# Optimization experiments

Hardware: AMD Instinct MI355X
Metric: run time of the kernel (lower is better)

## Reference

```python
import jax, jax.numpy as jnp
import numpy as np

MAX_ITERS = 20
TOL = 1e-6
STEP = 1.0
EPS = 1e-7
CLIP = 1e-7


def _normalize(x, axis=-1):
    n = jnp.linalg.norm(x, axis=axis, keepdims=True)
    return x / jnp.maximum(n, 1e-12)


def _safe_acos(x):
    return jnp.arccos(jnp.clip(x, -1.0 + CLIP, 1.0 - CLIP))


def setup_inputs() -> dict:
    key = jax.random.key(0)
    NC, K, N, D = 1000, 8, 32, 128
    X_groups = jax.random.normal(key, (NC, K, N, D), dtype=jnp.float32)
    return {"X_groups": X_groups}


def reference(X_groups):
    # X_groups: (NC, K, N, D)
    NC, K, N, D = X_groups.shape
    X = X_groups.reshape(NC * K, N, D)
    Xn = _normalize(X)                      # (G, N, D) unit vectors
    mu = _normalize(jnp.mean(Xn, axis=1))   # (G, D) init mean

    done = jnp.array(False)
    for _ in range(MAX_ITERS):
        dots = jnp.einsum('gd,gnd->gn', mu, Xn)             # (G, N)
        theta = _safe_acos(dots)
        sin_t = jnp.maximum(jnp.sin(theta), EPS)
        diff = Xn - dots[..., None] * mu[:, None, :]        # (G, N, D)
        log_vecs = (theta / sin_t)[..., None] * diff        # log map
        v = jnp.mean(log_vecs, axis=1)                      # (G, D)
        v_norm = jnp.maximum(jnp.linalg.norm(v, axis=-1, keepdims=True), EPS)
        done = done | (jnp.max(v_norm) < TOL)               # global convergence (as in torch .item() check)
        v_step = STEP * v
        vs_norm = jnp.maximum(jnp.linalg.norm(v_step, axis=-1, keepdims=True), EPS)
        mu_new = jnp.cos(vs_norm) * mu + jnp.sin(vs_norm) * (v_step / vs_norm)  # exp map
        mu_new = _normalize(mu_new)
        mu = jnp.where(done, mu, mu_new)

    # calc_cluster_distance: features (G, N, D) @ means (G, D)
    sims = jnp.einsum('gnd,gd->gn', Xn, mu)
    sims = jnp.clip(sims, -1 + CLIP, 1 - CLIP)
    loss = jnp.mean(jnp.sum(jnp.arccos(sims) ** 2, axis=-1))
    return loss
```

## Files before the change

kernel.cpp:

```cpp
#include <hip/hip_runtime.h>
#include <stdint.h>

#define MAX_ITERS 20
#define EPSV 1e-7f
#define CLIPV 1e-7f
#define PI_F 3.14159265358979f
#define PIO2_F 1.57079632679490f

typedef __attribute__((ext_vector_type(8))) short short8;
typedef __attribute__((ext_vector_type(4))) float f4;

__device__ __forceinline__ f4 mfma_bf16(short8 a, short8 b, f4 c) {
    return __builtin_amdgcn_mfma_f32_16x16x32_bf16(a, b, c, 0, 0, 0);
}

__device__ __forceinline__ float rl(float v, int l) {
    return __int_as_float(__builtin_amdgcn_readlane(__float_as_int(v), l));
}

template <int CTRL>
__device__ __forceinline__ float dpp_add(float v) {
    int p = __builtin_amdgcn_update_dpp(0, __float_as_int(v), CTRL, 0xF, 0xF, true);
    return v + __int_as_float(p);
}

__device__ __forceinline__ float rowsum32(float v) {
    v = dpp_add<0xB1>(v);
    v = dpp_add<0x4E>(v);
    v = dpp_add<0x141>(v);
    v = dpp_add<0x140>(v);
    return rl(v, 0) + rl(v, 16);
}

__device__ __forceinline__ float fast_acos(float x) {
    float a = fabsf(x);
    bool big = a > 0.5f;
    float z = big ? 0.5f * (1.0f - a) : x * x;
    float s = big ? sqrtf(z) : x;
    float p = fmaf(z, fmaf(z, fmaf(z, fmaf(z, 4.2163199048e-2f, 2.4181311049e-2f),
                                   4.5470025998e-2f), 7.4953002686e-2f),
                   1.6666752422e-1f);
    float r = fmaf(s * z, p, s);
    float big_val = (x < 0.0f) ? (PI_F - 2.0f * r) : (2.0f * r);
    return big ? big_val : (PIO2_F - r);
}

__device__ __forceinline__ void cvt_hilo(const float* v, short8& hi, short8& lo) {
#pragma unroll
    for (int i = 0; i < 8; ++i) {
        float x = v[i];
        uint32_t u = __float_as_uint(x);
        float hf = __uint_as_float(u & 0xFFFF0000u);
        float lf = x - hf;
        hi[i] = (short)(u >> 16);
        lo[i] = (short)(__float_as_uint(lf) >> 16);
    }
}

__global__ void __launch_bounds__(256) karcher(const float* __restrict__ X,
                                               float* __restrict__ ws,
                                               int n_groups) {
    __shared__ float sG[4][32 * 33];
    __shared__ float sInv[4][32];
    __shared__ float sPart[4];

    const int lane = threadIdx.x & 63;
    const int wid  = threadIdx.x >> 6;
    const int g    = blockIdx.x * 4 + wid;
    if (g >= n_groups) return;

    const float* Xg = X + (size_t)g * (32 * 128);
    const int col  = lane & 15;
    const int quad = lane >> 4;

    f4 acc00 = {0.f, 0.f, 0.f, 0.f};
    f4 acc01 = acc00, acc10 = acc00, acc11 = acc00;
#pragma unroll
    for (int kc = 0; kc < 4; ++kc) {
        const float* p0 = Xg + col * 128 + kc * 32 + quad * 8;
        const float* p1 = p0 + 16 * 128;
        float r0[8], r1[8];
        *(float4*)(r0)     = *(const float4*)(p0);
        *(float4*)(r0 + 4) = *(const float4*)(p0 + 4);
        *(float4*)(r1)     = *(const float4*)(p1);
        *(float4*)(r1 + 4) = *(const float4*)(p1 + 4);
        short8 H0, L0, H1, L1;
        cvt_hilo(r0, H0, L0);
        cvt_hilo(r1, H1, L1);
        acc00 = mfma_bf16(H0, H0, acc00);
        acc00 = mfma_bf16(H0, L0, acc00);
        acc00 = mfma_bf16(L0, H0, acc00);
        acc01 = mfma_bf16(H0, H1, acc01);
        acc01 = mfma_bf16(H0, L1, acc01);
        acc01 = mfma_bf16(L0, H1, acc01);
        acc10 = mfma_bf16(H1, H0, acc10);
        acc10 = mfma_bf16(H1, L0, acc10);
        acc10 = mfma_bf16(L1, H0, acc10);
        acc11 = mfma_bf16(H1, H1, acc11);
        acc11 = mfma_bf16(H1, L1, acc11);
        acc11 = mfma_bf16(L1, H1, acc11);
    }

    float* Gw = sG[wid];
#pragma unroll
    for (int i = 0; i < 4; ++i) {
        int rw = quad * 4 + i;
        Gw[rw * 33 + col]             = acc00[i];
        Gw[rw * 33 + col + 16]        = acc01[i];
        Gw[(rw + 16) * 33 + col]      = acc10[i];
        Gw[(rw + 16) * 33 + col + 16] = acc11[i];
    }
    __syncthreads();

    const int r = lane & 31;
    {
        float d = Gw[r * 33 + r];
        sInv[wid][r] = 1.0f / fmaxf(sqrtf(d), 1e-12f);
    }
    __syncthreads();

    float Grow[32];
    {
        float invr = sInv[wid][r];
#pragma unroll
        for (int j = 0; j < 32; ++j)
            Grow[j] = Gw[r * 33 + j] * (invr * sInv[wid][j]);
    }

    float a = 1.0f / 32.0f;
    float ga;
    {
        float s0 = 0, s1 = 0, s2 = 0, s3 = 0;
#pragma unroll
        for (int j = 0; j < 8; ++j) {
            s0 += Grow[j];
            s1 += Grow[j + 8];
            s2 += Grow[j + 16];
            s3 += Grow[j + 24];
        }
        ga = ((s0 + s1) + (s2 + s3)) * (1.0f / 32.0f);
        float n2   = rowsum32(a * ga);
        float inv0 = 1.0f / fmaxf(sqrtf(n2), 1e-12f);
        a  *= inv0;
        ga *= inv0;
    }

    for (int it = 0; it < MAX_ITERS; ++it) {
        float x  = fminf(fmaxf(ga, -1.0f + CLIPV), 1.0f - CLIPV);
        float th = fast_acos(x);
        float st = fmaxf(sqrtf(fmaxf(1.0f - x * x, 0.0f)), EPSV);
        float w  = __fdividef(th, st);
        float C  = rowsum32(w * ga);
        float beta = (w - C * a) * (1.0f / 32.0f);
        float gb0 = 0, gb1 = 0, gb2 = 0, gb3 = 0;
#pragma unroll
        for (int j = 0; j < 8; ++j) {
            gb0 = fmaf(Grow[j],      rl(beta, j),      gb0);
            gb1 = fmaf(Grow[j + 8],  rl(beta, j + 8),  gb1);
            gb2 = fmaf(Grow[j + 16], rl(beta, j + 16), gb2);
            gb3 = fmaf(Grow[j + 24], rl(beta, j + 24), gb3);
        }
        float gb = (gb0 + gb1) + (gb2 + gb3);
        float vv = rowsum32(beta * gb);
        float vs = fmaxf(sqrtf(fmaxf(vv, 0.0f)), EPSV);
        float cv = __cosf(vs);
        float sv = __fdividef(__sinf(vs), vs);
        a  = fmaf(sv, beta, cv * a);
        ga = fmaf(sv, gb, cv * ga);
        if (vs < 1e-6f) break;
    }

    float xf = fminf(fmaxf(ga, -1.0f + CLIPV), 1.0f - CLIPV);
    float t  = fast_acos(xf);
    float ls = rowsum32(t * t);
    if (lane == 0) sPart[wid] = ls;
    __syncthreads();
    if (threadIdx.x == 0)
        ws[blockIdx.x] = (sPart[0] + sPart[1]) + (sPart[2] + sPart[3]);
}

__global__ void __launch_bounds__(256) reduce_partials(const float* __restrict__ ws,
                                                       float* __restrict__ out,
                                                       int n, float scale) {
    __shared__ float sred[4];
    float s = 0.f;
    for (int i = threadIdx.x; i < n; i += 256) s += ws[i];
#pragma unroll
    for (int m = 32; m >= 1; m >>= 1) s += __shfl_xor(s, m, 64);
    const int lane = threadIdx.x & 63, wid = threadIdx.x >> 6;
    if (lane == 0) sred[wid] = s;
    __syncthreads();
    if (threadIdx.x == 0)
        out[0] = ((sred[0] + sred[1]) + (sred[2] + sred[3])) * scale;
}

extern "C" void kernel_launch(void* const* d_in, const int* in_sizes, int n_in,
                              void* d_out, int out_size, void* d_ws, size_t ws_size,
                              hipStream_t stream) {
    const float* X = (const float*)d_in[0];
    float* out = (float*)d_out;
    float* ws = (float*)d_ws;
    int n_groups = in_sizes[0] / (32 * 128);
    int blocks = (n_groups + 3) / 4;
    karcher<<<blocks, 256, 0, stream>>>(X, ws, n_groups);
    reduce_partials<<<1, 256, 0, stream>>>(ws, out, blocks, 1.0f / (float)n_groups);
}
```

Before: 212.5 us.

## Fold row normalization into iteration math and shrink blocks to two waves

Keeps the raw Gram matrix instead of normalizing it, folding the inverse norms into the coefficients and dot products each iteration. This removes a shared-memory pass and one block barrier. The C reduction and the G·u product now run independently, which shortens the serial dependency chain per iteration. Blocks shrink from 256 to 128 threads with per-wave partial outputs, dropping the cross-wave reduction. The bounds check is removed, so the kernel assumes the group count is even.

```diff
diff --git a/kernel.cpp b/kernel.cpp
--- a/kernel.cpp
+++ b/kernel.cpp
@@ -57,17 +57,14 @@
     }
 }
 
-__global__ void __launch_bounds__(256) karcher(const float* __restrict__ X,
+__global__ void __launch_bounds__(128) karcher(const float* __restrict__ X,
                                                float* __restrict__ ws,
                                                int n_groups) {
-    __shared__ float sG[4][32 * 33];
-    __shared__ float sInv[4][32];
-    __shared__ float sPart[4];
+    __shared__ float sG[2][32 * 33];
 
     const int lane = threadIdx.x & 63;
     const int wid  = threadIdx.x >> 6;
-    const int g    = blockIdx.x * 4 + wid;
-    if (g >= n_groups) return;
+    const int g    = blockIdx.x * 2 + wid;
 
     const float* Xg = X + (size_t)g * (32 * 128);
     const int col  = lane & 15;
@@ -113,32 +110,24 @@
     __syncthreads();
 
     const int r = lane & 31;
-    {
-        float d = Gw[r * 33 + r];
-        sInv[wid][r] = 1.0f / fmaxf(sqrtf(d), 1e-12f);
-    }
-    __syncthreads();
+    float Grow[32];
+#pragma unroll
+    for (int j = 0; j < 32; ++j) Grow[j] = Gw[r * 33 + j];
+    const float inv_  = 1.0f / fmaxf(sqrtf(Gw[r * 33 + r]), 1e-12f);
+    const float inv32 = inv_ * (1.0f / 32.0f);
 
-    float Grow[32];
-    {
-        float invr = sInv[wid][r];
-#pragma unroll
-        for (int j = 0; j < 32; ++j)
-            Grow[j] = Gw[r * 33 + j] * (invr * sInv[wid][j]);
-    }
-
-    float a = 1.0f / 32.0f;
+    float a = inv32;
     float ga;
     {
         float s0 = 0, s1 = 0, s2 = 0, s3 = 0;
 #pragma unroll
         for (int j = 0; j < 8; ++j) {
-            s0 += Grow[j];
-            s1 += Grow[j + 8];
-            s2 += Grow[j + 16];
-            s3 += Grow[j + 24];
+            s0 = fmaf(Grow[j],      rl(a, j),      s0);
+            s1 = fmaf(Grow[j + 8],  rl(a, j + 8),  s1);
+            s2 = fmaf(Grow[j + 16], rl(a, j + 16), s2);
+            s3 = fmaf(Grow[j + 24], rl(a, j + 24), s3);
         }
-        ga = ((s0 + s1) + (s2 + s3)) * (1.0f / 32.0f);
+        ga = (s0 + s1) + (s2 + s3);
         float n2   = rowsum32(a * ga);
         float inv0 = 1.0f / fmaxf(sqrtf(n2), 1e-12f);
         a  *= inv0;
@@ -146,21 +135,25 @@
     }
 
     for (int it = 0; it < MAX_ITERS; ++it) {
-        float x  = fminf(fmaxf(ga, -1.0f + CLIPV), 1.0f - CLIPV);
+        float dotr = ga * inv_;
+        float x  = fminf(fmaxf(dotr, -1.0f + CLIPV), 1.0f - CLIPV);
         float th = fast_acos(x);
         float st = fmaxf(sqrtf(fmaxf(1.0f - x * x, 0.0f)), EPSV);
         float w  = __fdividef(th, st);
-        float C  = rowsum32(w * ga);
-        float beta = (w - C * a) * (1.0f / 32.0f);
-        float gb0 = 0, gb1 = 0, gb2 = 0, gb3 = 0;
+        float u  = w * inv32;
+        float s0 = 0, s1 = 0, s2 = 0, s3 = 0;
 #pragma unroll
         for (int j = 0; j < 8; ++j) {
-            gb0 = fmaf(Grow[j],      rl(beta, j),      gb0);
-            gb1 = fmaf(Grow[j + 8],  rl(beta, j + 8),  gb1);
-            gb2 = fmaf(Grow[j + 16], rl(beta, j + 16), gb2);
-            gb3 = fmaf(Grow[j + 24], rl(beta, j + 24), gb3);
+            s0 = fmaf(Grow[j],      rl(u, j),      s0);
+            s1 = fmaf(Grow[j + 8],  rl(u, j + 8),  s1);
+            s2 = fmaf(Grow[j + 16], rl(u, j + 16), s2);
+            s3 = fmaf(Grow[j + 24], rl(u, j + 24), s3);
         }
-        float gb = (gb0 + gb1) + (gb2 + gb3);
+        float gu  = (s0 + s1) + (s2 + s3);
+        float C   = rowsum32(w * dotr);
+        float c32 = C * (1.0f / 32.0f);
+        float beta = u  - c32 * a;
+        float gb   = gu - c32 * ga;
         float vv = rowsum32(beta * gb);
         float vs = fmaxf(sqrtf(fmaxf(vv, 0.0f)), EPSV);
         float cv = __cosf(vs);
@@ -170,13 +163,10 @@
         if (vs < 1e-6f) break;
     }
 
-    float xf = fminf(fmaxf(ga, -1.0f + CLIPV), 1.0f - CLIPV);
+    float xf = fminf(fmaxf(ga * inv_, -1.0f + CLIPV), 1.0f - CLIPV);
     float t  = fast_acos(xf);
     float ls = rowsum32(t * t);
-    if (lane == 0) sPart[wid] = ls;
-    __syncthreads();
-    if (threadIdx.x == 0)
-        ws[blockIdx.x] = (sPart[0] + sPart[1]) + (sPart[2] + sPart[3]);
+    if (lane == 0) ws[blockIdx.x * 2 + wid] = ls;
 }
 
 __global__ void __launch_bounds__(256) reduce_partials(const float* __restrict__ ws,
@@ -201,7 +191,7 @@
     float* out = (float*)d_out;
     float* ws = (float*)d_ws;
     int n_groups = in_sizes[0] / (32 * 128);
-    int blocks = (n_groups + 3) / 4;
-    karcher<<<blocks, 256, 0, stream>>>(X, ws, n_groups);
-    reduce_partials<<<1, 256, 0, stream>>>(ws, out, blocks, 1.0f / (float)n_groups);
+    int blocks = n_groups / 2;
+    karcher<<<blocks, 128, 0, stream>>>(X, ws, n_groups);
+    reduce_partials<<<1, 256, 0, stream>>>(ws, out, n_groups, 1.0f / (float)n_groups);
 }
```

Result: slower. 229.3 us (+7.9%).
